# Performance work log

Hardware: AMD Instinct MI355X
Metric: run time of the kernel (lower is better)

Reference implementation:

```python
import jax, jax.numpy as jnp
import numpy as np

E = 800_000      # number of edges
DIN = 128        # in_channels
DMID = 256       # mid_channels
DOUT = 128       # output_channels
V = 50_000       # number of vertices (segments)


def setup_inputs() -> dict:
    key = jax.random.key(0)
    k1, k2, k3, k4, k5 = jax.random.split(key, 5)
    x = jax.random.normal(k1, (E, DIN), dtype=jnp.float32)
    vertex_id = jax.random.randint(k2, (E,), 0, V)
    W1 = jax.random.normal(k3, (DIN, DMID), dtype=jnp.float32) * (1.0 / np.sqrt(DIN))
    b1 = jax.random.normal(k4, (DMID,), dtype=jnp.float32) * 0.01
    W2 = jax.random.normal(k5, (DIN + DMID, DOUT), dtype=jnp.float32) * (1.0 / np.sqrt(DIN + DMID))
    return {"x": x, "vertex_id": vertex_id, "W1": W1, "b1": b1, "W2": W2, "num_vertices": V}


def reference(x, vertex_id, W1, b1, W2, num_vertices):
    # first_process: Linear(DIN -> DMID)                        (E, DMID)
    z = x @ W1 + b1
    # aggregator: scatter_max over vertex segments              (V, DMID)
    z_max = jax.ops.segment_max(z, vertex_id, num_segments=num_vertices)
    # formatter: index_select gather back to edges              (E, DMID)
    z_vertex = jnp.take(z_max, vertex_id, axis=0)
    # merger: concat along feature dim                          (E, DIN+DMID)
    z_merged = jnp.concatenate([x, z_vertex], axis=-1)
    # second_process: Linear(DIN+DMID -> DOUT, bias=False)      (E, DOUT)
    return z_merged @ W2
```

## Files before the change

### kernel.cpp

```cpp
#include <hip/hip_runtime.h>

#define DIN   128
#define DMID  256
#define DOUT  128
#define VNUM  50000

typedef __attribute__((ext_vector_type(8))) __bf16 bf16x8;
typedef __attribute__((ext_vector_type(4))) float  f32x4;

static __device__ __forceinline__ unsigned short b16(float f) {
  union { __bf16 b; unsigned short u; } r; r.b = (__bf16)f; return r.u;
}
static __device__ __forceinline__ unsigned pk2(float lo, float hi) {
  union { __bf16 b[2]; unsigned u; } r;
  r.b[0] = (__bf16)lo; r.b[1] = (__bf16)hi;
  return r.u;
}
static __device__ __forceinline__ unsigned unflip_bits(unsigned m) {
  unsigned mask = ((int)m < 0) ? 0x80000000u : 0xFFFFFFFFu;
  return m ^ mask;
}
static __device__ __forceinline__ unsigned flip32_from16(unsigned m) {
  return (m << 16) | ((m & 0x8000u) ? 0u : 0xFFFFu);
}

__global__ __launch_bounds__(256) void k_zero(uint4* __restrict__ p, int n16) {
  const int stride = gridDim.x * 256;
  const uint4 z = {0u, 0u, 0u, 0u};
  for (int i = blockIdx.x * 256 + threadIdx.x; i < n16; i += stride) p[i] = z;
}

__global__ void k_hist(const int* __restrict__ vid, int* __restrict__ counts, int E) {
  int i = blockIdx.x * blockDim.x + threadIdx.x;
  if (i < E) atomicAdd(counts + vid[i], 1);
}

__global__ __launch_bounds__(256) void k_scan_red(
    const int* __restrict__ cnt, int* __restrict__ bsum, int V) {
  __shared__ int ws[4];
  const int i = blockIdx.x * 256 + threadIdx.x;
  int c = (i < V) ? cnt[i] : 0;
#pragma unroll
  for (int d = 1; d < 64; d <<= 1) c += __shfl_xor(c, d);
  if ((threadIdx.x & 63) == 0) ws[threadIdx.x >> 6] = c;
  __syncthreads();
  if (threadIdx.x == 0) bsum[blockIdx.x] = ws[0] + ws[1] + ws[2] + ws[3];
}

__global__ __launch_bounds__(256) void k_scan_top(int* __restrict__ bsum, int nb) {
  __shared__ int ws[4];
  const int tid = threadIdx.x, lane = tid & 63, wv = tid >> 6;
  int c = (tid < nb) ? bsum[tid] : 0;
  int s = c;
#pragma unroll
  for (int d = 1; d < 64; d <<= 1) {
    int u = __shfl_up(s, d, 64);
    if (lane >= d) s += u;
  }
  if (lane == 63) ws[wv] = s;
  __syncthreads();
  int off = 0;
  for (int k = 0; k < wv; ++k) off += ws[k];
  if (tid < nb) bsum[tid] = off + (s - c);
}

__global__ __launch_bounds__(256) void k_scan_fix(
    int* __restrict__ cursor, const int* __restrict__ bsum, int V) {
  __shared__ int ws[4];
  const int i = blockIdx.x * 256 + threadIdx.x;
  const int lane = threadIdx.x & 63, wv = threadIdx.x >> 6;
  int c = (i < V) ? cursor[i] : 0;
  int s = c;
#pragma unroll
  for (int d = 1; d < 64; d <<= 1) {
    int u = __shfl_up(s, d, 64);
    if (lane >= d) s += u;
  }
  if (lane == 63) ws[wv] = s;
  __syncthreads();
  int off = bsum[blockIdx.x];
  for (int k = 0; k < wv; ++k) off += ws[k];
  if (i < V) cursor[i] = off + (s - c);
}

__global__ void k_scatter(const int* __restrict__ vid, int* __restrict__ cursor,
                          int* __restrict__ sorted, int E) {
  int i = blockIdx.x * blockDim.x + threadIdx.x;
  if (i < E) {
    int v = vid[i];
    int p = atomicAdd(cursor + v, 1);
    sorted[p] = i;
  }
}

__global__ __launch_bounds__(512) void k_gemm1_max(
    const float* __restrict__ x, const int* __restrict__ vid,
    const int* __restrict__ sorted, const float* __restrict__ W1,
    const float* __restrict__ b1, unsigned* __restrict__ zu, int ntiles) {
  __shared__ unsigned short lx[64 * 136];
  __shared__ unsigned short zt[256 * 70];
  __shared__ int lvid[2][64];

  const int tid  = threadIdx.x;
  const int lane = tid & 63;
  const int w    = tid >> 6;
  const int l15  = lane & 15;
  const int l4   = lane >> 4;
  const int row8 = tid >> 3;
  const int s8   = tid & 7;
  const int G    = gridDim.x;

  bf16x8 bfrag[4][2];
  float  bias[2];
#pragma unroll
  for (int ni = 0; ni < 2; ++ni) {
    const int col = w * 32 + ni * 16 + l15;
    bias[ni] = b1[col];
#pragma unroll
    for (int kk = 0; kk < 4; ++kk) {
      union { bf16x8 v; unsigned short u[8]; } tmp;
#pragma unroll
      for (int j = 0; j < 8; ++j)
        tmp.u[j] = b16(W1[(kk * 32 + l4 * 8 + j) * DMID + col]);
      bfrag[kk][ni] = tmp.v;
    }
  }

  const int t0 = blockIdx.x;
  if (t0 >= ntiles) return;

  {
    if (tid < 64) lvid[0][tid] = vid[sorted[t0 * 64 + tid]];
    const int eid = sorted[t0 * 64 + row8];
    const float4* src =
        reinterpret_cast<const float4*>(x + (size_t)eid * DIN + s8 * 16);
#pragma unroll
    for (int i = 0; i < 4; ++i) {
      float4 v = src[i];
      uint2 o = { pk2(v.x, v.y), pk2(v.z, v.w) };
      *reinterpret_cast<uint2*>(&lx[row8 * 136 + s8 * 16 + i * 4]) = o;
    }
  }
  __syncthreads();

  int cur = 0;
  for (int t = t0; t < ntiles; t += G, cur ^= 1) {
    const int tn = t + G;
    const bool more = (tn < ntiles);
    int eidN = 0, sidN = 0;
    if (more) {
      eidN = sorted[tn * 64 + row8];
      if (tid < 64) sidN = sorted[tn * 64 + tid];
    }

    const int myv = lvid[cur][lane];
    const int nv  = (lane == 63) ? (myv ^ 1) : lvid[cur][lane + 1];
    const unsigned long long emask = __ballot(myv != nv);
    const bool contOpen = (lvid[cur][31] == lvid[cur][32]);

    f32x4 acc[4][2];
#pragma unroll
    for (int mi = 0; mi < 4; ++mi)
#pragma unroll
      for (int ni = 0; ni < 2; ++ni)
        acc[mi][ni] = (f32x4){bias[ni], bias[ni], bias[ni], bias[ni]};
#pragma unroll
    for (int kk = 0; kk < 4; ++kk) {
      bf16x8 a[4];
#pragma unroll
      for (int mi = 0; mi < 4; ++mi)
        a[mi] = *reinterpret_cast<const bf16x8*>(
            &lx[(mi * 16 + l15) * 136 + kk * 32 + l4 * 8]);
#pragma unroll
      for (int mi = 0; mi < 4; ++mi)
#pragma unroll
        for (int ni = 0; ni < 2; ++ni)
          acc[mi][ni] = __builtin_amdgcn_mfma_f32_16x16x32_bf16(
              a[mi], bfrag[kk][ni], acc[mi][ni], 0, 0, 0);
    }

    {
      unsigned* ztw = reinterpret_cast<unsigned*>(zt);
#pragma unroll
      for (int ni = 0; ni < 2; ++ni) {
        const int col = w * 32 + ni * 16 + l15;
        const int cb  = col * 35 + l4 * 2;
#pragma unroll
        for (int mi = 0; mi < 4; ++mi)
#pragma unroll
          for (int p = 0; p < 2; ++p) {
            unsigned tpk = pk2(acc[mi][ni][2 * p], acc[mi][ni][2 * p + 1]);
            unsigned mflip = 0x80008000u + ((tpk >> 15) & 0x00010001u) * 0x7FFFu;
            ztw[cb + mi * 8 + p] = tpk ^ mflip;
          }
      }
    }
    __syncthreads();

    float4 x0, x1, x2, x3;
    int vN = 0;
    if (more) {
      const float4* src =
          reinterpret_cast<const float4*>(x + (size_t)eidN * DIN + s8 * 16);
      x0 = src[0]; x1 = src[1]; x2 = src[2]; x3 = src[3];
      if (tid < 64) vN = vid[sidN];
    }

    {
      const int col = tid & 255;
      const int h   = tid >> 8;
      const unsigned* zc = reinterpret_cast<const unsigned*>(&zt[col * 70 + h * 32]);
      unsigned curm = 0;
      bool first = true;
#pragma unroll
      for (int p = 0; p < 16; ++p) {
        const unsigned pr = zc[p];
#pragma unroll
        for (int j = 0; j < 2; ++j) {
          const unsigned val = j ? (pr >> 16) : (pr & 0xFFFFu);
          curm = val > curm ? val : curm;
          const int row = h * 32 + p * 2 + j;
          if ((emask >> row) & 1) {
            const int v = lvid[cur][row];
            const unsigned enc = flip32_from16(curm);
            unsigned* ad = zu + (size_t)v * DMID + col;
            if (row == 63 || (first && (h == 0 || contOpen))) atomicMax(ad, enc);
            else *ad = enc;
            curm = 0; first = false;
          }
        }
      }
      if (h == 0 && !((emask >> 31) & 1)) {
        const int v = lvid[cur][31];
        atomicMax(zu + (size_t)v * DMID + col, flip32_from16(curm));
      }
    }

    if (more) {
      uint2 o0 = { pk2(x0.x, x0.y), pk2(x0.z, x0.w) };
      uint2 o1 = { pk2(x1.x, x1.y), pk2(x1.z, x1.w) };
      uint2 o2 = { pk2(x2.x, x2.y), pk2(x2.z, x2.w) };
      uint2 o3 = { pk2(x3.x, x3.y), pk2(x3.z, x3.w) };
      unsigned short* dst = &lx[row8 * 136 + s8 * 16];
      *reinterpret_cast<uint2*>(dst + 0)  = o0;
      *reinterpret_cast<uint2*>(dst + 4)  = o1;
      *reinterpret_cast<uint2*>(dst + 8)  = o2;
      *reinterpret_cast<uint2*>(dst + 12) = o3;
      if (tid < 64) lvid[cur ^ 1][tid] = vN;
    }
    __syncthreads();
  }
}

__global__ __launch_bounds__(256) void k_ymm(
    const unsigned* __restrict__ zu, const float* __restrict__ W2,
    float* __restrict__ Y, int ntiles) {
  extern __shared__ unsigned short sm[];
  unsigned short* w2bt = sm;
  unsigned short* za   = sm + 128 * 264;

  const int tid  = threadIdx.x;
  const int lane = tid & 63;
  const int w    = tid >> 6;
  const int wr   = w >> 1, wc = w & 1;
  const int l15  = lane & 15, l4 = lane >> 4;

  {
    const int n = tid & 127, kh = tid >> 7;
    for (int k = kh * 128; k < kh * 128 + 128; ++k)
      w2bt[n * 264 + k] = b16(W2[(size_t)(DIN + k) * DOUT + n]);
  }
  __syncthreads();

  for (int t = blockIdx.x; t < ntiles; t += gridDim.x) {
    {
      const int row = tid >> 2, q = tid & 3;
      const int v = t * 64 + row;
      unsigned short* dz = &za[row * 264 + q * 64];
      if (v < VNUM) {
        const uint4* sz = reinterpret_cast<const uint4*>(zu + (size_t)v * DMID + q * 64);
#pragma unroll
        for (int i = 0; i < 16; ++i) {
          uint4 m = sz[i];
          ushort4 o = { (unsigned short)(unflip_bits(m.x) >> 16),
                        (unsigned short)(unflip_bits(m.y) >> 16),
                        (unsigned short)(unflip_bits(m.z) >> 16),
                        (unsigned short)(unflip_bits(m.w) >> 16) };
          *reinterpret_cast<ushort4*>(dz + i * 4) = o;
        }
      } else {
        ushort4 zo = {0, 0, 0, 0};
#pragma unroll
        for (int i = 0; i < 16; ++i) *reinterpret_cast<ushort4*>(dz + i * 4) = zo;
      }
    }
    __syncthreads();

    f32x4 acc[2][4];
#pragma unroll
    for (int mi = 0; mi < 2; ++mi)
#pragma unroll
      for (int ni = 0; ni < 4; ++ni) acc[mi][ni] = (f32x4){0.f, 0.f, 0.f, 0.f};

#pragma unroll
    for (int kk = 0; kk < 8; ++kk) {
      bf16x8 a[2], b[4];
#pragma unroll
      for (int mi = 0; mi < 2; ++mi)
        a[mi] = *reinterpret_cast<const bf16x8*>(
            &za[(wr * 32 + mi * 16 + l15) * 264 + kk * 32 + l4 * 8]);
#pragma unroll
      for (int ni = 0; ni < 4; ++ni)
        b[ni] = *reinterpret_cast<const bf16x8*>(
            &w2bt[(wc * 64 + ni * 16 + l15) * 264 + kk * 32 + l4 * 8]);
#pragma unroll
      for (int mi = 0; mi < 2; ++mi)
#pragma unroll
        for (int ni = 0; ni < 4; ++ni)
          acc[mi][ni] = __builtin_amdgcn_mfma_f32_16x16x32_bf16(
              a[mi], b[ni], acc[mi][ni], 0, 0, 0);
    }

#pragma unroll
    for (int mi = 0; mi < 2; ++mi)
#pragma unroll
      for (int r = 0; r < 4; ++r) {
        const int v = t * 64 + wr * 32 + mi * 16 + l4 * 4 + r;
        if (v < VNUM) {
          float* o = Y + (size_t)v * DOUT + wc * 64 + l15;
#pragma unroll
          for (int ni = 0; ni < 4; ++ni) o[ni * 16] = acc[mi][ni][r];
        }
      }
    __syncthreads();
  }
}

__global__ __launch_bounds__(256, 3) void k_gemm2(
    const float* __restrict__ x, const int* __restrict__ vid,
    const float* __restrict__ W2, const float* __restrict__ Y,
    float* __restrict__ out, int ntiles) {
  __shared__ unsigned short w2at[128 * 136];
  __shared__ unsigned short lx[64 * 136];
  __shared__ int lvid[64];

  const int tid  = threadIdx.x;
  const int lane = tid & 63;
  const int w    = tid >> 6;
  const int wr   = w >> 1, wc = w & 1;
  const int l15  = lane & 15, l4 = lane >> 4;

  {
    const int n = tid & 127, kh = tid >> 7;
    for (int k = kh * 64; k < kh * 64 + 64; ++k)
      w2at[n * 136 + k] = b16(W2[(size_t)k * DOUT + n]);
  }
  __syncthreads();

  for (int t = blockIdx.x; t < ntiles; t += gridDim.x) {
    {
      const int row = tid >> 2, q = tid & 3;
      const float4* sx =
          reinterpret_cast<const float4*>(x + (size_t)(t * 64 + row) * DIN + q * 32);
#pragma unroll
      for (int i = 0; i < 8; ++i) {
        float4 v = sx[i];
        uint2 o = { pk2(v.x, v.y), pk2(v.z, v.w) };
        *reinterpret_cast<uint2*>(&lx[row * 136 + q * 32 + i * 4]) = o;
      }
      if (tid < 64) lvid[tid] = vid[t * 64 + tid];
    }
    __syncthreads();

    float yv[2][4][4];
#pragma unroll
    for (int mi = 0; mi < 2; ++mi)
#pragma unroll
      for (int r = 0; r < 4; ++r) {
        const int row = wr * 32 + mi * 16 + l4 * 4 + r;
        const float* Yr = Y + (size_t)lvid[row] * DOUT + wc * 64 + l15;
#pragma unroll
        for (int ni = 0; ni < 4; ++ni) yv[mi][r][ni] = Yr[ni * 16];
      }

    f32x4 acc[2][4];
#pragma unroll
    for (int mi = 0; mi < 2; ++mi)
#pragma unroll
      for (int ni = 0; ni < 4; ++ni) acc[mi][ni] = (f32x4){0.f, 0.f, 0.f, 0.f};

#pragma unroll
    for (int kk = 0; kk < 4; ++kk) {
      bf16x8 a[2], b[4];
#pragma unroll
      for (int mi = 0; mi < 2; ++mi)
        a[mi] = *reinterpret_cast<const bf16x8*>(
            &lx[(wr * 32 + mi * 16 + l15) * 136 + kk * 32 + l4 * 8]);
#pragma unroll
      for (int ni = 0; ni < 4; ++ni)
        b[ni] = *reinterpret_cast<const bf16x8*>(
            &w2at[(wc * 64 + ni * 16 + l15) * 136 + kk * 32 + l4 * 8]);
#pragma unroll
      for (int mi = 0; mi < 2; ++mi)
#pragma unroll
        for (int ni = 0; ni < 4; ++ni)
          acc[mi][ni] = __builtin_amdgcn_mfma_f32_16x16x32_bf16(
              a[mi], b[ni], acc[mi][ni], 0, 0, 0);
    }

#pragma unroll
    for (int mi = 0; mi < 2; ++mi)
#pragma unroll
      for (int r = 0; r < 4; ++r) {
        const int row = wr * 32 + mi * 16 + l4 * 4 + r;
        float* o = out + (size_t)(t * 64 + row) * DOUT + wc * 64 + l15;
#pragma unroll
        for (int ni = 0; ni < 4; ++ni) o[ni * 16] = acc[mi][ni][r] + yv[mi][r][ni];
      }
    __syncthreads();
  }
}

extern "C" void kernel_launch(void* const* d_in, const int* in_sizes, int n_in,
                              void* d_out, int out_size, void* d_ws, size_t ws_size,
                              hipStream_t stream) {
  const float* x   = (const float*)d_in[0];
  const int*   vid = (const int*)d_in[1];
  const float* W1  = (const float*)d_in[2];
  const float* b1  = (const float*)d_in[3];
  const float* W2  = (const float*)d_in[4];
  float* out = (float*)d_out;

  const int E = in_sizes[1];
  const int ntiles = E / 64;
  const int ntY = (VNUM + 63) / 64;
  const int nb = (VNUM + 255) / 256;

  char* ws = (char*)d_ws;
  size_t off = 0;
  unsigned* zu = (unsigned*)(ws + off); off += (size_t)VNUM * DMID * 4;
  int* cnt     = (int*)(ws + off);      off += (size_t)VNUM * 4;
  int* sorted  = (int*)(ws + off);      off += (size_t)E * 4;
  float* Y     = (float*)(ws + off);    off += (size_t)VNUM * DOUT * 4;
  int* bsum    = (int*)(ws + off);      off += 4096;

  const int n16 = (int)(((size_t)VNUM * DMID * 4 + VNUM * 4) / 16);
  k_zero<<<2048, 256, 0, stream>>>((uint4*)zu, n16);

  k_hist<<<(E + 255) / 256, 256, 0, stream>>>(vid, cnt, E);
  k_scan_red<<<nb, 256, 0, stream>>>(cnt, bsum, VNUM);
  k_scan_top<<<1, 256, 0, stream>>>(bsum, nb);
  k_scan_fix<<<nb, 256, 0, stream>>>(cnt, bsum, VNUM);
  k_scatter<<<(E + 255) / 256, 256, 0, stream>>>(vid, cnt, sorted, E);

  k_gemm1_max<<<2048, 512, 0, stream>>>(x, vid, sorted, W1, b1, zu, ntiles);

  const int smY = (128 * 264 + 64 * 264) * sizeof(unsigned short);
  hipFuncSetAttribute((const void*)k_ymm,
                      hipFuncAttributeMaxDynamicSharedMemorySize, smY);
  k_ymm<<<782, 256, smY, stream>>>(zu, W2, Y, ntY);

  k_gemm2<<<768, 256, 0, stream>>>(x, vid, W2, Y, out, ntiles);
}
```

Baseline: 623.8 us.

## Deepen x-row prefetch in gemm1_max and use LDS-only barriers

```diff
diff --git a/kernel.cpp b/kernel.cpp
--- a/kernel.cpp
+++ b/kernel.cpp
@@ -23,6 +23,14 @@
 static __device__ __forceinline__ unsigned flip32_from16(unsigned m) {
   return (m << 16) | ((m & 0x8000u) ? 0u : 0xFFFFu);
 }
+
+#define LBAR() do {                                            \
+    __builtin_amdgcn_sched_barrier(0);                         \
+    asm volatile("s_waitcnt lgkmcnt(0)" ::: "memory");         \
+    __builtin_amdgcn_sched_barrier(0);                         \
+    __builtin_amdgcn_s_barrier();                              \
+    __builtin_amdgcn_sched_barrier(0);                         \
+  } while (0)
 
 __global__ __launch_bounds__(256) void k_zero(uint4* __restrict__ p, int n16) {
   const int stride = gridDim.x * 256;
@@ -141,16 +149,30 @@
       *reinterpret_cast<uint2*>(&lx[row8 * 136 + s8 * 16 + i * 4]) = o;
     }
   }
+  int eidN = 0, sidN = 0;
+  bool moreP = (t0 + G) < ntiles;
+  if (moreP) {
+    eidN = sorted[(t0 + G) * 64 + row8];
+    if (tid < 64) sidN = sorted[(t0 + G) * 64 + tid];
+  }
   __syncthreads();
 
   int cur = 0;
   for (int t = t0; t < ntiles; t += G, cur ^= 1) {
-    const int tn = t + G;
-    const bool more = (tn < ntiles);
-    int eidN = 0, sidN = 0;
-    if (more) {
-      eidN = sorted[tn * 64 + row8];
-      if (tid < 64) sidN = sorted[tn * 64 + tid];
+    const bool more1 = (t + G) < ntiles;
+    float4 x0, x1, x2, x3;
+    int vN = 0;
+    if (more1) {
+      const float4* src =
+          reinterpret_cast<const float4*>(x + (size_t)eidN * DIN + s8 * 16);
+      x0 = src[0]; x1 = src[1]; x2 = src[2]; x3 = src[3];
+      if (tid < 64) vN = vid[sidN];
+    }
+    const bool more2 = (t + 2 * G) < ntiles;
+    int eidN2 = 0, sidN2 = 0;
+    if (more2) {
+      eidN2 = sorted[(t + 2 * G) * 64 + row8];
+      if (tid < 64) sidN2 = sorted[(t + 2 * G) * 64 + tid];
     }
 
     const int myv = lvid[cur][lane];
@@ -195,16 +217,21 @@
           }
       }
     }
-    __syncthreads();
-
-    float4 x0, x1, x2, x3;
-    int vN = 0;
-    if (more) {
-      const float4* src =
-          reinterpret_cast<const float4*>(x + (size_t)eidN * DIN + s8 * 16);
-      x0 = src[0]; x1 = src[1]; x2 = src[2]; x3 = src[3];
-      if (tid < 64) vN = vid[sidN];
-    }
+    LBAR();
+
+    if (more1) {
+      uint2 o0 = { pk2(x0.x, x0.y), pk2(x0.z, x0.w) };
+      uint2 o1 = { pk2(x1.x, x1.y), pk2(x1.z, x1.w) };
+      uint2 o2 = { pk2(x2.x, x2.y), pk2(x2.z, x2.w) };
+      uint2 o3 = { pk2(x3.x, x3.y), pk2(x3.z, x3.w) };
+      unsigned short* dst = &lx[row8 * 136 + s8 * 16];
+      *reinterpret_cast<uint2*>(dst + 0)  = o0;
+      *reinterpret_cast<uint2*>(dst + 4)  = o1;
+      *reinterpret_cast<uint2*>(dst + 8)  = o2;
+      *reinterpret_cast<uint2*>(dst + 12) = o3;
+      if (tid < 64) lvid[cur ^ 1][tid] = vN;
+    }
+    __builtin_amdgcn_sched_barrier(0);
 
     {
       const int col = tid & 255;
@@ -235,20 +262,8 @@
         atomicMax(zu + (size_t)v * DMID + col, flip32_from16(curm));
       }
     }
-
-    if (more) {
-      uint2 o0 = { pk2(x0.x, x0.y), pk2(x0.z, x0.w) };
-      uint2 o1 = { pk2(x1.x, x1.y), pk2(x1.z, x1.w) };
-      uint2 o2 = { pk2(x2.x, x2.y), pk2(x2.z, x2.w) };
-      uint2 o3 = { pk2(x3.x, x3.y), pk2(x3.z, x3.w) };
-      unsigned short* dst = &lx[row8 * 136 + s8 * 16];
-      *reinterpret_cast<uint2*>(dst + 0)  = o0;
-      *reinterpret_cast<uint2*>(dst + 4)  = o1;
-      *reinterpret_cast<uint2*>(dst + 8)  = o2;
-      *reinterpret_cast<uint2*>(dst + 12) = o3;
-      if (tid < 64) lvid[cur ^ 1][tid] = vN;
-    }
-    __syncthreads();
+    eidN = eidN2; sidN = sidN2;
+    LBAR();
   }
 }
 
@@ -453,7 +468,7 @@
   k_scan_fix<<<nb, 256, 0, stream>>>(cnt, bsum, VNUM);
   k_scatter<<<(E + 255) / 256, 256, 0, stream>>>(vid, cnt, sorted, E);
 
-  k_gemm1_max<<<2048, 512, 0, stream>>>(x, vid, sorted, W1, b1, zu, ntiles);
+  k_gemm1_max<<<512, 512, 0, stream>>>(x, vid, sorted, W1, b1, zu, ntiles);
 
   const int smY = (128 * 264 + 64 * 264) * sizeof(unsigned short);
   hipFuncSetAttribute((const void*)k_ymm,
```

After: 586.8 us. -5.9%, faster.
